# Kernel optimization log

Measured on AMD Instinct MI355X. Metric: run time of the kernel, lower is better.

## Reference

```python
import jax, jax.numpy as jnp
import numpy as np

B, T = 1024, 128
LEN_VOCAB, IPD_VOCAB = 1500, 256
LEN_EB, IPD_EB = 64, 64
RNN_IN, HIDDEN, LABELS = 128, 512, 100


def setup_inputs() -> dict:
    key = jax.random.key(0)
    ks = jax.random.split(key, 11)
    std = 1.0 / np.sqrt(HIDDEN)

    def u(k, shape, s):
        return jax.random.uniform(k, shape, jnp.float32, -s, s)

    return {
        "x": jax.random.randint(ks[0], (B, T, 2), 0, 256, dtype=jnp.int64),
        "len_emb": jax.random.normal(ks[1], (LEN_VOCAB, LEN_EB), jnp.float32),
        "ipd_emb": jax.random.normal(ks[2], (IPD_VOCAB, IPD_EB), jnp.float32),
        "fc1_w": u(ks[3], (RNN_IN, LEN_EB + IPD_EB), 1.0 / np.sqrt(LEN_EB + IPD_EB)),
        "fc1_b": u(ks[4], (RNN_IN,), 1.0 / np.sqrt(LEN_EB + IPD_EB)),
        "x2h_w": u(ks[5], (HIDDEN, RNN_IN), std),
        "x2h_b": u(ks[6], (HIDDEN,), std),
        "h2h_w": u(ks[7], (HIDDEN, HIDDEN), std),
        "h2h_b": u(ks[8], (HIDDEN,), std),
        "fc2_w": u(ks[9], (LABELS, HIDDEN), 1.0 / np.sqrt(HIDDEN)),
        "fc2_b": u(ks[10], (LABELS,), 1.0 / np.sqrt(HIDDEN)),
    }


def reference(x, len_emb, ipd_emb, fc1_w, fc1_b, x2h_w, x2h_b, h2h_w, h2h_b, fc2_w, fc2_b):
    # Embedding lookups: [B, T, 64] each -> concat [B, T, 128]
    feats = jnp.concatenate([len_emb[x[:, :, 0]], ipd_emb[x[:, :, 1]]], axis=-1)
    # fc1 then precompute the x2h part of the recurrence for all timesteps
    r = feats @ fc1_w.T + fc1_b                       # [B, T, RNN_IN]
    xin = r @ x2h_w.T + x2h_b                         # [B, T, HIDDEN]
    xin_t = jnp.swapaxes(xin, 0, 1)                   # [T, B, HIDDEN]

    def step(h, xt):
        h = jnp.tanh(xt + h @ h2h_w.T + h2h_b)
        return h, None

    h0 = jnp.zeros((x.shape[0], h2h_w.shape[0]), dtype=xin.dtype)
    h_last, _ = jax.lax.scan(step, h0, xin_t)
    # eval mode: dropout is identity
    return h_last @ fc2_w.T + fc2_b                   # [B, LABELS]
```

## Files before the change

kernel.cpp:

```cpp
#include <hip/hip_runtime.h>

#define B_SZ 1024
#define T_SZ 128
#define HID 512
#define LAB 100

#define OFF_XC    0u
#define OFF_WH    262144u
#define OFF_FC2   786432u
#define OFF_FC2B  888832u
#define OFF_WEFFT 889344u
#define OFF_BEFF  1151488u
#define OFF_ELEN  1153536u
#define OFF_EIPD  1415680u
#define WS_NEED   1677824u

typedef __attribute__((ext_vector_type(8))) short short8;
typedef __attribute__((ext_vector_type(8))) unsigned short us8;
typedef __attribute__((ext_vector_type(4))) float float4v;
typedef __attribute__((ext_vector_type(4))) unsigned short us4;
typedef __attribute__((ext_vector_type(8))) __bf16 bf8_t;
typedef unsigned long long ull;

__device__ __attribute__((aligned(16))) unsigned char g_blob[WS_NEED];

__device__ __forceinline__ float bf2f(unsigned short u) {
    union { unsigned int i; float f; } z; z.i = ((unsigned int)u) << 16; return z.f;
}
__device__ __forceinline__ unsigned short f2bf(float f) {
    union { float f; unsigned int i; } z; z.f = f;
    unsigned int r = z.i + 0x7FFFu + ((z.i >> 16) & 1u);
    return (unsigned short)(r >> 16);
}
__device__ __forceinline__ float4v mfma16(short8 a, short8 b, float4v c) {
    return __builtin_amdgcn_mfma_f32_16x16x32_bf16(
        __builtin_bit_cast(bf8_t, a), __builtin_bit_cast(bf8_t, b), c, 0, 0, 0);
}

__launch_bounds__(256)
__global__ void k1_kernel(const float* __restrict__ fc1_f, const float* __restrict__ fc1b_f,
                          const float* __restrict__ x2h_f, const float* __restrict__ x2hb_f,
                          const float* __restrict__ h2hb_f,
                          float* __restrict__ wefft, float* __restrict__ beff) {
    const int tid = threadIdx.x;
    if (blockIdx.x < 64) {
        int gid = blockIdx.x * 256 + tid;
        int n  = gid >> 5;
        int k0 = (gid & 31) * 4;
        const float* xr = x2h_f + n * 128;
        float a0 = 0.f, a1 = 0.f, a2 = 0.f, a3 = 0.f;
#pragma unroll 4
        for (int j = 0; j < 128; j++) {
            float xv = xr[j];
            float4v fv = *(const float4v*)(fc1_f + j * 128 + k0);
            a0 += xv * fv[0]; a1 += xv * fv[1];
            a2 += xv * fv[2]; a3 += xv * fv[3];
        }
        wefft[(k0 + 0) * 512 + n] = a0;
        wefft[(k0 + 1) * 512 + n] = a1;
        wefft[(k0 + 2) * 512 + n] = a2;
        wefft[(k0 + 3) * 512 + n] = a3;
        return;
    }
    int tg = (blockIdx.x - 64) * 256 + tid;
    float s = x2hb_f[tg] + h2hb_f[tg];
    const float4v* xr = (const float4v*)(x2h_f + tg * 128);
    const float4v* bb = (const float4v*)fc1b_f;
    for (int j = 0; j < 32; j++) {
        float4v a = xr[j], b = bb[j];
        s += a[0] * b[0] + a[1] * b[1] + a[2] * b[2] + a[3] * b[3];
    }
    beff[tg] = s;
}

__launch_bounds__(256)
__global__ void k2_kernel(const float* __restrict__ wefft, const float* __restrict__ beff,
                          const float* __restrict__ len_f, const float* __restrict__ ipd_f,
                          const int* __restrict__ xi, unsigned char* __restrict__ xc,
                          const float* __restrict__ h2h_f, const float* __restrict__ fc2_f,
                          const float* __restrict__ fc2b_f,
                          unsigned short* __restrict__ elen, unsigned short* __restrict__ eipd,
                          unsigned short* __restrict__ o_wh, unsigned short* __restrict__ o_fc2,
                          float* __restrict__ o_fc2b) {
    const int tid = threadIdx.x;
    if (blockIdx.x < 256) {
        int grp = blockIdx.x * 256 + tid;
        int tab = grp >> 15;
        int g2  = grp & 32767;
        int v   = g2 >> 7;
        int nq  = (g2 & 127) * 4;
        const float* emb = (tab ? ipd_f : len_f) + v * 64;
        const float* wt  = wefft + tab * 64 * 512 + nq;
        float a0 = 0.f, a1 = 0.f, a2 = 0.f, a3 = 0.f;
#pragma unroll 8
        for (int k = 0; k < 64; k++) {
            float e = emb[k];
            float4v w = *(const float4v*)(wt + k * 512);
            a0 += e * w[0]; a1 += e * w[1]; a2 += e * w[2]; a3 += e * w[3];
        }
        if (tab) {
            float4v b4 = *(const float4v*)&beff[nq];
            a0 += b4[0]; a1 += b4[1]; a2 += b4[2]; a3 += b4[3];
        }
        int nt = (nq >> 4) & 3, qq = (nq >> 2) & 3;
        int p0 = (nq & ~63) + ((nt >> 1) << 5) + qq * 8 + ((nt & 1) << 2);
        us4 o = { f2bf(a0), f2bf(a1), f2bf(a2), f2bf(a3) };
        unsigned short* dst = tab ? eipd : elen;
        *(us4*)&dst[v * 512 + p0] = o;
        return;
    }
    if (blockIdx.x < 512) {
        __shared__ int is64;
        if (tid == 0) {
            int nz = 0;
            for (int j = 1; j < 64; j += 2) nz |= xi[j];
            is64 = (nz == 0) ? 1 : 0;
        }
        __syncthreads();
        const int n = B_SZ * T_SZ * 2;
        const int i64 = is64;
        for (int i = (blockIdx.x - 256) * 256 + tid; i < n; i += 256 * 256) {
            int v = i64 ? xi[2 * i] : xi[i];
            v = v < 0 ? 0 : (v > 255 ? 255 : v);
            int b = i >> 8, r = i & 255, t = r >> 1, c = r & 1;
            xc[t * 2048 + b * 2 + c] = (unsigned char)v;
        }
        return;
    }
    const int NW4 = 65536;
    const int NF4 = 12800;
    int gid = (blockIdx.x - 512) * 256 + tid;
    if (gid < NW4) {
        float4v a = *(const float4v*)(h2h_f + gid * 4);
        us4 o = { f2bf(a[0]), f2bf(a[1]), f2bf(a[2]), f2bf(a[3]) };
        *(us4*)&o_wh[gid * 4] = o;
    } else if (gid < NW4 + NF4) {
        int j = gid - NW4;
        float4v a = *(const float4v*)(fc2_f + j * 4);
        us4 o = { f2bf(a[0]), f2bf(a[1]), f2bf(a[2]), f2bf(a[3]) };
        *(us4*)&o_fc2[j * 4] = o;
    } else if (gid < NW4 + NF4 + 100) {
        int j = gid - NW4 - NF4;
        o_fc2b[j] = fc2b_f[j];
    }
}

__launch_bounds__(512, 2)
__global__ void rnn_kernel(const unsigned short* __restrict__ w_wh,
                           const unsigned char* __restrict__ w_xc,
                           const unsigned short* __restrict__ w_elen,
                           const unsigned short* __restrict__ w_eipd,
                           const unsigned short* __restrict__ w_fc2,
                           const float* __restrict__ w_fc2b,
                           float* __restrict__ out) {
    extern __shared__ unsigned short sm2[];
    unsigned short* sA = sm2;
    unsigned short* sH = sm2 + 65536;

    const int tid  = threadIdx.x;
    const int wv   = tid >> 6;
    const int ln   = tid & 63;
    const int mcol = ln & 15;
    const int q    = ln >> 4;
    const int g    = blockIdx.x;
    const int b0   = g * 16;
    const int n0   = wv * 64;

    for (int it = 0; it < 16; it++) {
        int chunk = it * 512 + tid;
        int r = chunk >> 4, c = chunk & 15;
        uint4 v = *(const uint4*)(w_wh + r * 512 + 384 + c * 8);
        *(uint4*)&sA[r * 128 + ((c ^ (r & 15)) & 15) * 8] = v;
    }
    {
        uint4 z = {0, 0, 0, 0};
        *(uint4*)&sH[tid * 8] = z;
        *(uint4*)&sH[(512 + tid) * 8] = z;
    }
    short8 whr[4][12];
#pragma unroll
    for (int nt = 0; nt < 4; nt++)
#pragma unroll
        for (int kt = 0; kt < 12; kt++)
            whr[nt][kt] = *(const short8*)(w_wh + (n0 + nt * 16 + mcol) * 512 + kt * 32 + q * 8);

    const int qlo = (q ^ (mcol & 3)) * 8;
    int ej[4];
#pragma unroll
    for (int j = 0; j < 4; j++)
        ej[j] = ((j * 4) ^ (mcol & 12)) * 8;
    const int base_b = mcol * 512 + qlo;
    const int fbase  = (n0 + mcol) * 128 + qlo;
    int hw_off[4];
#pragma unroll
    for (int nt = 0; nt < 4; nt++) {
        int n = n0 + nt * 16 + q * 4;
        hw_off[nt] = mcol * 512 + (((n >> 3) ^ mcol) & 63) * 8 + (n & 7);
    }

    const int xb2  = (b0 + mcol) * 2;
    const int ecol = n0 + q * 8;
    us8 tL0, tL1, tI0, tI1;
    {
        unsigned int i0 = *(const unsigned short*)&w_xc[xb2];
        const unsigned short* eL = w_elen + (i0 & 255u) * 512 + ecol;
        const unsigned short* eI = w_eipd + (i0 >> 8) * 512 + ecol;
        tL0 = *(const us8*)eL;  tL1 = *(const us8*)(eL + 32);
        tI0 = *(const us8*)eI;  tI1 = *(const us8*)(eI + 32);
    }
    unsigned int idxP = *(const unsigned short*)&w_xc[2048 + xb2];

    __syncthreads();

    for (int t = 0; t < T_SZ; t++) {
        const unsigned short* hRd = sH + ((t & 1) << 13);
        unsigned short* hWr = sH + (((t + 1) & 1) << 13);

        float4v acc[4];
#pragma unroll
        for (int r = 0; r < 4; r++) {
            acc[0][r] = bf2f(tL0[r])     + bf2f(tI0[r]);
            acc[1][r] = bf2f(tL0[4 + r]) + bf2f(tI0[4 + r]);
            acc[2][r] = bf2f(tL1[r])     + bf2f(tI1[r]);
            acc[3][r] = bf2f(tL1[4 + r]) + bf2f(tI1[4 + r]);
        }
        if (t + 1 < T_SZ) {
            const unsigned short* eL = w_elen + (idxP & 255u) * 512 + ecol;
            const unsigned short* eI = w_eipd + (idxP >> 8) * 512 + ecol;
            tL0 = *(const us8*)eL;  tL1 = *(const us8*)(eL + 32);
            tI0 = *(const us8*)eI;  tI1 = *(const us8*)(eI + 32);
            if (t + 2 < T_SZ)
                idxP = *(const unsigned short*)&w_xc[(t + 2) * 2048 + xb2];
        }

#pragma unroll
        for (int kt = 0; kt < 12; kt++) {
            short8 bh = *(const short8*)&hRd[base_b + ej[kt & 3] + (kt >> 2) * 128];
#pragma unroll
            for (int nt = 0; nt < 4; nt++)
                acc[nt] = mfma16(whr[nt][kt], bh, acc[nt]);
        }
#pragma unroll
        for (int j = 0; j < 4; j++) {
            short8 bh = *(const short8*)&hRd[base_b + ej[j] + 384];
#pragma unroll
            for (int nt = 0; nt < 4; nt++) {
                short8 fa = *(const short8*)&sA[fbase + nt * 2048 + ej[j]];
                acc[nt] = mfma16(fa, bh, acc[nt]);
            }
        }

#pragma unroll
        for (int nt = 0; nt < 4; nt++) {
            unsigned short o[4];
#pragma unroll
            for (int r = 0; r < 4; r++) {
                float e  = __expf(2.0f * acc[nt][r]);
                float th = 1.0f - 2.0f * __builtin_amdgcn_rcpf(e + 1.0f);
                o[r] = f2bf(th);
            }
            us4 v4 = { o[0], o[1], o[2], o[3] };
            *(us4*)&hWr[hw_off[nt]] = v4;
        }
        __syncthreads();
    }

    unsigned short* hF = sH;

    if (wv < 7) {
        int lA = wv * 16 + mcol; if (lA > 99) lA = 99;
        float4v a2 = {0.f, 0.f, 0.f, 0.f};
#pragma unroll
        for (int kt = 0; kt < 16; kt++) {
            short8 fa = *(const short8*)(w_fc2 + lA * 512 + kt * 32 + q * 8);
            short8 bh = *(const short8*)&hF[base_b + ej[kt & 3] + (kt >> 2) * 128];
            a2 = mfma16(fa, bh, a2);
        }
#pragma unroll
        for (int r = 0; r < 4; r++) {
            int l = wv * 16 + q * 4 + r;
            if (l < 100) out[(b0 + mcol) * 100 + l] = a2[r] + w_fc2b[l];
        }
    }
}

extern "C" void kernel_launch(void* const* d_in, const int* in_sizes, int n_in,
                              void* d_out, int out_size, void* d_ws, size_t ws_size,
                              hipStream_t stream) {
    unsigned char* base = (unsigned char*)d_ws;
    if (ws_size < (size_t)WS_NEED) {
        void* p = nullptr;
        hipGetSymbolAddress(&p, HIP_SYMBOL(g_blob));
        base = (unsigned char*)p;
    }
    unsigned char*  w_xc    = base + OFF_XC;
    unsigned short* w_wh    = (unsigned short*)(base + OFF_WH);
    unsigned short* w_fc2   = (unsigned short*)(base + OFF_FC2);
    float*          w_fc2b  = (float*)(base + OFF_FC2B);
    float*          w_wefft = (float*)(base + OFF_WEFFT);
    float*          w_beff  = (float*)(base + OFF_BEFF);
    unsigned short* w_elen  = (unsigned short*)(base + OFF_ELEN);
    unsigned short* w_eipd  = (unsigned short*)(base + OFF_EIPD);

    static bool attr_set = false;
    if (!attr_set) {
        hipFuncSetAttribute((const void*)rnn_kernel,
                            hipFuncAttributeMaxDynamicSharedMemorySize, 163840);
        attr_set = true;
    }

    k1_kernel<<<66, 256, 0, stream>>>(
        (const float*)d_in[3], (const float*)d_in[4],
        (const float*)d_in[5], (const float*)d_in[6], (const float*)d_in[8],
        w_wefft, w_beff);
    k2_kernel<<<819, 256, 0, stream>>>(
        w_wefft, w_beff,
        (const float*)d_in[1], (const float*)d_in[2],
        (const int*)d_in[0], w_xc,
        (const float*)d_in[7], (const float*)d_in[9], (const float*)d_in[10],
        w_elen, w_eipd, w_wh, w_fc2, w_fc2b);
    rnn_kernel<<<64, 512, 163840, stream>>>(
        w_wh, w_xc, w_elen, w_eipd, w_fc2, w_fc2b, (float*)d_out);
}
```

Measured before the change: 356.1 us.

## Stream last K-slice of recurrent weights from pre-packed global buffer instead of LDS

```diff
diff --git a/kernel.cpp b/kernel.cpp
--- a/kernel.cpp
+++ b/kernel.cpp
@@ -13,7 +13,8 @@
 #define OFF_BEFF  1151488u
 #define OFF_ELEN  1153536u
 #define OFF_EIPD  1415680u
-#define WS_NEED   1677824u
+#define OFF_WHP   1677824u
+#define WS_NEED   1808896u
 
 typedef __attribute__((ext_vector_type(8))) short short8;
 typedef __attribute__((ext_vector_type(8))) unsigned short us8;
@@ -81,7 +82,8 @@
                           const float* __restrict__ fc2b_f,
                           unsigned short* __restrict__ elen, unsigned short* __restrict__ eipd,
                           unsigned short* __restrict__ o_wh, unsigned short* __restrict__ o_fc2,
-                          float* __restrict__ o_fc2b) {
+                          float* __restrict__ o_fc2b,
+                          unsigned short* __restrict__ o_whp) {
     const int tid = threadIdx.x;
     if (blockIdx.x < 256) {
         int grp = blockIdx.x * 256 + tid;
@@ -127,26 +129,44 @@
         }
         return;
     }
-    const int NW4 = 65536;
-    const int NF4 = 12800;
-    int gid = (blockIdx.x - 512) * 256 + tid;
-    if (gid < NW4) {
-        float4v a = *(const float4v*)(h2h_f + gid * 4);
-        us4 o = { f2bf(a[0]), f2bf(a[1]), f2bf(a[2]), f2bf(a[3]) };
-        *(us4*)&o_wh[gid * 4] = o;
-    } else if (gid < NW4 + NF4) {
-        int j = gid - NW4;
-        float4v a = *(const float4v*)(fc2_f + j * 4);
-        us4 o = { f2bf(a[0]), f2bf(a[1]), f2bf(a[2]), f2bf(a[3]) };
-        *(us4*)&o_fc2[j * 4] = o;
-    } else if (gid < NW4 + NF4 + 100) {
-        int j = gid - NW4 - NF4;
-        o_fc2b[j] = fc2b_f[j];
+    if (blockIdx.x < 819) {
+        const int NW4 = 65536;
+        const int NF4 = 12800;
+        int gid = (blockIdx.x - 512) * 256 + tid;
+        if (gid < NW4) {
+            float4v a = *(const float4v*)(h2h_f + gid * 4);
+            us4 o = { f2bf(a[0]), f2bf(a[1]), f2bf(a[2]), f2bf(a[3]) };
+            *(us4*)&o_wh[gid * 4] = o;
+        } else if (gid < NW4 + NF4) {
+            int j = gid - NW4;
+            float4v a = *(const float4v*)(fc2_f + j * 4);
+            us4 o = { f2bf(a[0]), f2bf(a[1]), f2bf(a[2]), f2bf(a[3]) };
+            *(us4*)&o_fc2[j * 4] = o;
+        } else if (gid < NW4 + NF4 + 100) {
+            int j = gid - NW4 - NF4;
+            o_fc2b[j] = fc2b_f[j];
+        }
+        return;
+    }
+    {
+        int gid = (blockIdx.x - 819) * 256 + tid;
+        int lnw = gid & 63;
+        int j   = (gid >> 6) & 3;
+        int nt  = (gid >> 8) & 3;
+        int wvp = gid >> 10;
+        int mcolp = lnw & 15, qp = lnw >> 4;
+        const float* s = h2h_f + (wvp * 64 + nt * 16 + mcolp) * 512 + (12 + j) * 32 + qp * 8;
+        float4v a = *(const float4v*)s;
+        float4v d = *(const float4v*)(s + 4);
+        us8 o = { f2bf(a[0]), f2bf(a[1]), f2bf(a[2]), f2bf(a[3]),
+                  f2bf(d[0]), f2bf(d[1]), f2bf(d[2]), f2bf(d[3]) };
+        *(us8*)&o_whp[gid * 8] = o;
     }
 }
 
 __launch_bounds__(512, 2)
 __global__ void rnn_kernel(const unsigned short* __restrict__ w_wh,
+                           const unsigned short* __restrict__ w_whp,
                            const unsigned char* __restrict__ w_xc,
                            const unsigned short* __restrict__ w_elen,
                            const unsigned short* __restrict__ w_eipd,
@@ -154,8 +174,7 @@
                            const float* __restrict__ w_fc2b,
                            float* __restrict__ out) {
     extern __shared__ unsigned short sm2[];
-    unsigned short* sA = sm2;
-    unsigned short* sH = sm2 + 65536;
+    unsigned short* sH = sm2;
 
     const int tid  = threadIdx.x;
     const int wv   = tid >> 6;
@@ -166,12 +185,6 @@
     const int b0   = g * 16;
     const int n0   = wv * 64;
 
-    for (int it = 0; it < 16; it++) {
-        int chunk = it * 512 + tid;
-        int r = chunk >> 4, c = chunk & 15;
-        uint4 v = *(const uint4*)(w_wh + r * 512 + 384 + c * 8);
-        *(uint4*)&sA[r * 128 + ((c ^ (r & 15)) & 15) * 8] = v;
-    }
     {
         uint4 z = {0, 0, 0, 0};
         *(uint4*)&sH[tid * 8] = z;
@@ -190,13 +203,13 @@
     for (int j = 0; j < 4; j++)
         ej[j] = ((j * 4) ^ (mcol & 12)) * 8;
     const int base_b = mcol * 512 + qlo;
-    const int fbase  = (n0 + mcol) * 128 + qlo;
     int hw_off[4];
 #pragma unroll
     for (int nt = 0; nt < 4; nt++) {
         int n = n0 + nt * 16 + q * 4;
         hw_off[nt] = mcol * 512 + (((n >> 3) ^ mcol) & 63) * 8 + (n & 7);
     }
+    const unsigned short* whp_t = w_whp + wv * 8192 + ln * 8;
 
     const int xb2  = (b0 + mcol) * 2;
     const int ecol = n0 + q * 8;
@@ -232,6 +245,10 @@
             if (t + 2 < T_SZ)
                 idxP = *(const unsigned short*)&w_xc[(t + 2) * 2048 + xb2];
         }
+        us8 fnx[4];
+#pragma unroll
+        for (int nt = 0; nt < 4; nt++)
+            fnx[nt] = *(const us8*)(whp_t + nt * 2048);
 
 #pragma unroll
         for (int kt = 0; kt < 12; kt++) {
@@ -242,12 +259,18 @@
         }
 #pragma unroll
         for (int j = 0; j < 4; j++) {
+            us8 fcur[4];
+#pragma unroll
+            for (int nt = 0; nt < 4; nt++) fcur[nt] = fnx[nt];
+            if (j < 3) {
+#pragma unroll
+                for (int nt = 0; nt < 4; nt++)
+                    fnx[nt] = *(const us8*)(whp_t + nt * 2048 + (j + 1) * 512);
+            }
             short8 bh = *(const short8*)&hRd[base_b + ej[j] + 384];
 #pragma unroll
-            for (int nt = 0; nt < 4; nt++) {
-                short8 fa = *(const short8*)&sA[fbase + nt * 2048 + ej[j]];
-                acc[nt] = mfma16(fa, bh, acc[nt]);
-            }
+            for (int nt = 0; nt < 4; nt++)
+                acc[nt] = mfma16(__builtin_bit_cast(short8, fcur[nt]), bh, acc[nt]);
         }
 
 #pragma unroll
@@ -301,11 +324,12 @@
     float*          w_beff  = (float*)(base + OFF_BEFF);
     unsigned short* w_elen  = (unsigned short*)(base + OFF_ELEN);
     unsigned short* w_eipd  = (unsigned short*)(base + OFF_EIPD);
+    unsigned short* w_whp   = (unsigned short*)(base + OFF_WHP);
 
     static bool attr_set = false;
     if (!attr_set) {
         hipFuncSetAttribute((const void*)rnn_kernel,
-                            hipFuncAttributeMaxDynamicSharedMemorySize, 163840);
+                            hipFuncAttributeMaxDynamicSharedMemorySize, 32768);
         attr_set = true;
     }
 
@@ -313,12 +337,12 @@
         (const float*)d_in[3], (const float*)d_in[4],
         (const float*)d_in[5], (const float*)d_in[6], (const float*)d_in[8],
         w_wefft, w_beff);
-    k2_kernel<<<819, 256, 0, stream>>>(
+    k2_kernel<<<851, 256, 0, stream>>>(
         w_wefft, w_beff,
         (const float*)d_in[1], (const float*)d_in[2],
         (const int*)d_in[0], w_xc,
         (const float*)d_in[7], (const float*)d_in[9], (const float*)d_in[10],
-        w_elen, w_eipd, w_wh, w_fc2, w_fc2b);
-    rnn_kernel<<<64, 512, 163840, stream>>>(
-        w_wh, w_xc, w_elen, w_eipd, w_fc2, w_fc2b, (float*)d_out);
-}
+        w_elen, w_eipd, w_wh, w_fc2, w_fc2b, w_whp);
+    rnn_kernel<<<64, 512, 32768, stream>>>(
+        w_wh, w_whp, w_xc, w_elen, w_eipd, w_fc2, w_fc2b, (float*)d_out);
+}
```

Result: slower. 697.1 us (+95.8%).
